# Kernel tuning notes

Hardware: AMD Instinct MI355X
Metric: run time of the kernel (lower is better)

## Reference

```python
import jax, jax.numpy as jnp
import numpy as np

N = 100000
DIM = 128
E = 3200000


def setup_inputs() -> dict:
    key = jax.random.key(0)
    k1, k2, k3, k4 = jax.random.split(key, 4)
    x = jax.random.normal(k1, (N, DIM), dtype=jnp.float32)
    edge_index = jax.random.randint(k2, (2, E), 0, N, dtype=jnp.int64)
    # GCNConv params: glorot-style weight [dim, dim], zero-init bias
    W = jax.random.normal(k3, (DIM, DIM), dtype=jnp.float32) * (1.0 / np.sqrt(DIM))
    b = jnp.zeros((DIM,), dtype=jnp.float32)
    return {"x": x, "edge_index": edge_index, "W": W, "b": b}


def gcn_conv(x, edge_index, W, b):
    n = x.shape[0]
    # add self-loops (PyG default add_self_loops=True)
    loop = jnp.arange(n, dtype=edge_index.dtype)
    row = jnp.concatenate([edge_index[0], loop])  # source
    col = jnp.concatenate([edge_index[1], loop])  # target (aggregation index)
    # symmetric normalization D^-1/2 (A+I) D^-1/2; degree counted on targets
    deg = jax.ops.segment_sum(jnp.ones_like(col, dtype=x.dtype), col, num_segments=n)
    dinv = jnp.where(deg > 0, jax.lax.rsqrt(deg), 0.0)
    norm = dinv[row] * dinv[col]  # [E+N]
    xw = x @ W  # dense transform first (dim small)
    msgs = xw[row] * norm[:, None]  # gather + scale
    out = jax.ops.segment_sum(msgs, col, num_segments=n)  # scatter-add
    return out + b


def reference(x, edge_index, W, b):
    # NOTE: original torch loop recomputes from the same x every iteration,
    # so the result equals a single relu(GCNConv(x, edge_index)).
    return jax.nn.relu(gcn_conv(x, edge_index, W, b))
```

## Files before the change

kernel.cpp:

```cpp
#include <hip/hip_runtime.h>

#define DIM 128
#define E_FIXED 3200000
#define BSH 7
#define BNODES 128
#define NB 784
#define BCAP 4864
#define NBLK 256
#define CAPH 2816

__device__ __forceinline__ float bflo(unsigned int w) { return __uint_as_float(w << 16); }
__device__ __forceinline__ float bfhi(unsigned int w) { return __uint_as_float(w & 0xffff0000u); }
__device__ __forceinline__ unsigned short f2bf(float f) {
    union { float f; unsigned int u; } c; c.f = f;
    unsigned int u = c.u + 0x7FFFu + ((c.u >> 16) & 1u);
    return (unsigned short)(u >> 16);
}

__global__ void detect_kernel(const int* __restrict__ edge, int force64, int* __restrict__ flag) {
    __shared__ int any_nonzero;
    if (threadIdx.x == 0) any_nonzero = 0;
    __syncthreads();
    if (edge[2 * threadIdx.x + 1] != 0) atomicOr(&any_nonzero, 1);
    __syncthreads();
    if (threadIdx.x == 0) *flag = force64 ? 1 : (any_nonzero ? 0 : 1);
}

__global__ __launch_bounds__(1024) void hist_kernel(const int* __restrict__ edge,
                                                    const int* __restrict__ flag,
                                                    int* __restrict__ hist_g, int E) {
    __shared__ int h[NB];
    const int tid = threadIdx.x;
    const int k = blockIdx.x;
    for (int b = tid; b < NB; b += 1024) h[b] = 0;
    __syncthreads();

    const int sh = *flag;
    const int cpb = (E + NBLK - 1) / NBLK;
    const int e0 = k * cpb;
    const int e1 = min(E, e0 + cpb);
    for (int e = e0 + tid; e < e1; e += 1024) {
        int c = edge[((size_t)(E + e)) << sh];
        atomicAdd(&h[c >> BSH], 1);
    }
    __syncthreads();
    for (int b = tid; b < NB; b += 1024) hist_g[(size_t)k * NB + b] = h[b];
}

__global__ __launch_bounds__(NBLK) void prefix_kernel(const int* __restrict__ hist_g,
                                                      int* __restrict__ pre_t,
                                                      int* __restrict__ total) {
    __shared__ int sc[2][NBLK];
    const int b = blockIdx.x;
    const int t = threadIdx.x;
    int v = hist_g[(size_t)t * NB + b];
    sc[0][t] = v;
    __syncthreads();
    int buf = 0;
#pragma unroll
    for (int off = 1; off < NBLK; off <<= 1) {
        sc[buf ^ 1][t] = sc[buf][t] + ((t >= off) ? sc[buf][t - off] : 0);
        buf ^= 1;
        __syncthreads();
    }
    pre_t[(size_t)b * NBLK + t] = sc[buf][t] - v;
    if (t == NBLK - 1) total[b] = sc[buf][t];
}

__global__ __launch_bounds__(512) void scatter_kernel(const int* __restrict__ edge,
                                                      const int* __restrict__ flag,
                                                      const int* __restrict__ pre_t,
                                                      int* __restrict__ bucketed, int E) {
    __shared__ int cur[NB];
    const int tid = threadIdx.x;
    const int k = blockIdx.x;
    for (int b = tid; b < NB; b += 512) cur[b] = pre_t[(size_t)b * NBLK + k];
    __syncthreads();

    const int sh = *flag;
    const int cpb = (E + NBLK - 1) / NBLK;
    const int e0 = k * cpb;
    const int e1 = min(E, e0 + cpb);
    for (int e = e0 + tid; e < e1; e += 512) {
        int r = edge[((size_t)e) << sh];
        int c = edge[((size_t)(E + e)) << sh];
        int b = c >> BSH;
        int pos = atomicAdd(&cur[b], 1);
        if (pos < BCAP)
            bucketed[(size_t)b * BCAP + pos] = (r << BSH) | (c & (BNODES - 1));
    }
}

__global__ __launch_bounds__(256) void degree_kernel(const int* __restrict__ bucketed,
                                                     const int* __restrict__ total,
                                                     int* __restrict__ deg, int n) {
    __shared__ int h[BNODES];
    const int b = blockIdx.x, t = threadIdx.x;
    if (t < BNODES) h[t] = 0;
    __syncthreads();
    const int m = min(total[b], BCAP);
    const int* seg = bucketed + (size_t)b * BCAP;
    for (int i = t; i < m; i += 256) atomicAdd(&h[seg[i] & (BNODES - 1)], 1);
    __syncthreads();
    int gnode = (b << BSH) + t;
    if (t < BNODES && gnode < n) deg[gnode] = h[t];
}

__global__ __launch_bounds__(256) void gemm_kernel(const float* __restrict__ x,
                                                   const float* __restrict__ W,
                                                   const int* __restrict__ deg,
                                                   unsigned short* __restrict__ xws, int n) {
    __shared__ float xs[64][132];
    const int tid = threadIdx.x;
    const int base = blockIdx.x * 64;
#pragma unroll
    for (int it = 0; it < 8; ++it) {
        int idx = it * 256 + tid;
        int r = idx >> 5;
        int k4 = idx & 31;
        int gr = base + r;
        float4 v = make_float4(0.f, 0.f, 0.f, 0.f);
        if (gr < n) v = ((const float4*)(x + (size_t)gr * DIM))[k4];
        *(float4*)&xs[r][k4 * 4] = v;
    }
    __syncthreads();

    const int j = tid & 31;
    const int g = tid >> 5;
    const float4* W4 = (const float4*)W;
    float acc[8][4];
#pragma unroll
    for (int t = 0; t < 8; ++t) { acc[t][0] = acc[t][1] = acc[t][2] = acc[t][3] = 0.f; }

    for (int k0 = 0; k0 < DIM; k0 += 4) {
        float4 w0 = W4[(size_t)(k0 + 0) * 32 + j];
        float4 w1 = W4[(size_t)(k0 + 1) * 32 + j];
        float4 w2 = W4[(size_t)(k0 + 2) * 32 + j];
        float4 w3 = W4[(size_t)(k0 + 3) * 32 + j];
#pragma unroll
        for (int t = 0; t < 8; ++t) {
            float4 xv = *(const float4*)&xs[g * 8 + t][k0];
            acc[t][0] = fmaf(xv.x, w0.x, fmaf(xv.y, w1.x, fmaf(xv.z, w2.x, fmaf(xv.w, w3.x, acc[t][0]))));
            acc[t][1] = fmaf(xv.x, w0.y, fmaf(xv.y, w1.y, fmaf(xv.z, w2.y, fmaf(xv.w, w3.y, acc[t][1]))));
            acc[t][2] = fmaf(xv.x, w0.z, fmaf(xv.y, w1.z, fmaf(xv.z, w2.z, fmaf(xv.w, w3.z, acc[t][2]))));
            acc[t][3] = fmaf(xv.x, w0.w, fmaf(xv.y, w1.w, fmaf(xv.z, w2.w, fmaf(xv.w, w3.w, acc[t][3]))));
        }
    }
#pragma unroll
    for (int t = 0; t < 8; ++t) {
        int gr = base + g * 8 + t;
        if (gr < n) {
            float dv = rsqrtf((float)(deg[gr] + 1));
            ushort4 o;
            o.x = f2bf(acc[t][0] * dv); o.y = f2bf(acc[t][1] * dv);
            o.z = f2bf(acc[t][2] * dv); o.w = f2bf(acc[t][3] * dv);
            *(ushort4*)&xws[(size_t)gr * DIM + j * 4] = o;
        }
    }
}

__device__ __forceinline__ void bf8_acc(uint4 u, float4& p, float4& r) {
    p.x += bflo(u.x); p.y += bfhi(u.x);
    p.z += bflo(u.y); p.w += bfhi(u.y);
    r.x += bflo(u.z); r.y += bfhi(u.z);
    r.z += bflo(u.w); r.w += bfhi(u.w);
}

__global__ __launch_bounds__(256) void agg_kernel(const unsigned short* __restrict__ xws,
                                                  const int* __restrict__ bucketed,
                                                  const int* __restrict__ total,
                                                  const int* __restrict__ deg,
                                                  const float* __restrict__ bias,
                                                  float* __restrict__ out, int n) {
    __shared__ int lds_csr[CAPH];
    __shared__ int hcur[64];
    __shared__ int sc[2][64];
    __shared__ int loff[65];
    __shared__ float sdn[64];
    __shared__ float sbias[DIM];

    const int tid = threadIdx.x;
    const int b = blockIdx.x >> 1;
    const int half = blockIdx.x & 1;
    const int m = min(total[b], BCAP);
    const int* seg = bucketed + (size_t)b * BCAP;
    const int base_node = (b << BSH) + half * 64;

    if (tid < 64) {
        int gn = base_node + tid;
        int d = (gn < n) ? deg[gn] : 0;
        sc[0][tid] = d;
        hcur[tid] = 0;
        sdn[tid] = rsqrtf((float)(d + 1));
    }
    if (tid < DIM) sbias[tid] = bias[tid];
    __syncthreads();
    int buf = 0;
#pragma unroll
    for (int off = 1; off < 64; off <<= 1) {
        if (tid < 64)
            sc[buf ^ 1][tid] = sc[buf][tid] + ((tid >= off) ? sc[buf][tid - off] : 0);
        buf ^= 1;
        __syncthreads();
    }
    if (tid < 64) loff[tid + 1] = sc[buf][tid];
    if (tid == 0) loff[0] = 0;
    __syncthreads();

    for (int i = tid; i < m; i += 256) {
        int v = seg[i];
        int loc = v & (BNODES - 1);
        if ((loc >> 6) == half) {
            int pos = atomicAdd(&hcur[loc & 63], 1);
            lds_csr[loff[loc & 63] + pos] = v >> BSH;
        }
    }
    __syncthreads();

    const int wave = tid >> 6, lane = tid & 63;
    const int q = lane >> 4;
    const int l16 = lane & 15;
    const int d0 = l16 * 8;

    for (int nl = wave * 16; nl < wave * 16 + 16; ++nl) {
        int gnode = base_node + nl;
        if (gnode >= n) break;
        int s = loff[nl], epos = loff[nl + 1];

        float4 a0 = make_float4(0.f, 0.f, 0.f, 0.f), a1 = a0, b0 = a0, b1 = a0;
        if (q == 0) {
            uint4 u = *(const uint4*)&xws[(size_t)gnode * DIM + d0];
            bf8_acc(u, a0, a1);
        }

        int e = s;
        for (; e + 16 <= epos; e += 16) {
            int r0 = lds_csr[e + q];
            int r1 = lds_csr[e + 4 + q];
            int r2 = lds_csr[e + 8 + q];
            int r3 = lds_csr[e + 12 + q];
            uint4 u0 = *(const uint4*)&xws[(size_t)r0 * DIM + d0];
            uint4 u1 = *(const uint4*)&xws[(size_t)r1 * DIM + d0];
            uint4 u2 = *(const uint4*)&xws[(size_t)r2 * DIM + d0];
            uint4 u3 = *(const uint4*)&xws[(size_t)r3 * DIM + d0];
            bf8_acc(u0, a0, a1);
            bf8_acc(u1, b0, b1);
            bf8_acc(u2, a0, a1);
            bf8_acc(u3, b0, b1);
        }
        for (; e + 4 <= epos; e += 4) {
            int r0 = lds_csr[e + q];
            uint4 u0 = *(const uint4*)&xws[(size_t)r0 * DIM + d0];
            bf8_acc(u0, a0, a1);
        }
        for (; e < epos; ++e) {
            if (q == 0) {
                int r = lds_csr[e];
                uint4 u = *(const uint4*)&xws[(size_t)r * DIM + d0];
                bf8_acc(u, a0, a1);
            }
        }

        float t0x = a0.x + b0.x, t0y = a0.y + b0.y, t0z = a0.z + b0.z, t0w = a0.w + b0.w;
        float t1x = a1.x + b1.x, t1y = a1.y + b1.y, t1z = a1.z + b1.z, t1w = a1.w + b1.w;
        t0x += __shfl_xor(t0x, 16); t0y += __shfl_xor(t0y, 16);
        t0z += __shfl_xor(t0z, 16); t0w += __shfl_xor(t0w, 16);
        t1x += __shfl_xor(t1x, 16); t1y += __shfl_xor(t1y, 16);
        t1z += __shfl_xor(t1z, 16); t1w += __shfl_xor(t1w, 16);
        t0x += __shfl_xor(t0x, 32); t0y += __shfl_xor(t0y, 32);
        t0z += __shfl_xor(t0z, 32); t0w += __shfl_xor(t0w, 32);
        t1x += __shfl_xor(t1x, 32); t1y += __shfl_xor(t1y, 32);
        t1z += __shfl_xor(t1z, 32); t1w += __shfl_xor(t1w, 32);

        float dn = sdn[nl];
        if (q == 0) {
            float4 sb = *(const float4*)&sbias[d0];
            float4 o;
            o.x = fmaxf(t0x * dn + sb.x, 0.f);
            o.y = fmaxf(t0y * dn + sb.y, 0.f);
            o.z = fmaxf(t0z * dn + sb.z, 0.f);
            o.w = fmaxf(t0w * dn + sb.w, 0.f);
            *(float4*)&out[(size_t)gnode * DIM + d0] = o;
        } else if (q == 1) {
            float4 sb = *(const float4*)&sbias[d0 + 4];
            float4 o;
            o.x = fmaxf(t1x * dn + sb.x, 0.f);
            o.y = fmaxf(t1y * dn + sb.y, 0.f);
            o.z = fmaxf(t1z * dn + sb.z, 0.f);
            o.w = fmaxf(t1w * dn + sb.w, 0.f);
            *(float4*)&out[(size_t)gnode * DIM + d0 + 4] = o;
        }
    }
}

extern "C" void kernel_launch(void* const* d_in, const int* in_sizes, int n_in,
                              void* d_out, int out_size, void* d_ws, size_t ws_size,
                              hipStream_t stream) {
    const float* x    = (const float*)d_in[0];
    const int*   edge = (const int*)d_in[1];
    const float* W    = (const float*)d_in[2];
    const float* bias = (const float*)d_in[3];
    float* out = (float*)d_out;

    const int n = in_sizes[0] / DIM;
    const int E = (in_sizes[1] == 4 * E_FIXED) ? E_FIXED : in_sizes[1] / 2;
    const int force64 = (in_sizes[1] == 4 * E_FIXED) ? 1 : 0;
    const int nbuck = (n + BNODES - 1) >> BSH;
    const int nhalf = (n + 63) / 64;

    char* p = (char*)d_ws;
    auto carve = [&](size_t bytes) { char* r = p; p += (bytes + 255) & ~(size_t)255; return (void*)r; };
    unsigned short* xws = (unsigned short*)carve((size_t)n * DIM * 2);
    int*   deg      = (int*)carve((size_t)n * 4);
    int*   flag     = (int*)carve(256);
    int*   hist_g   = (int*)carve((size_t)NBLK * NB * 4);
    int*   pre_t    = (int*)carve((size_t)NB * NBLK * 4);
    int*   total    = (int*)carve((size_t)NB * 4);
    int*   bucketed = (int*)carve((size_t)NB * BCAP * 4);

    detect_kernel<<<1, 128, 0, stream>>>(edge, force64, flag);
    hist_kernel<<<NBLK, 1024, 0, stream>>>(edge, flag, hist_g, E);
    prefix_kernel<<<NB, NBLK, 0, stream>>>(hist_g, pre_t, total);
    scatter_kernel<<<NBLK, 512, 0, stream>>>(edge, flag, pre_t, bucketed, E);
    degree_kernel<<<nbuck, 256, 0, stream>>>(bucketed, total, deg, n);
    gemm_kernel<<<(n + 63) / 64, 256, 0, stream>>>(x, W, deg, xws, n);
    agg_kernel<<<nhalf * 2, 256, 0, stream>>>(xws, bucketed, total, deg, bias, out, n);
}
```

Before: 230.8 us.

## Shrink buckets to 64 nodes, inline edge-width detection, software-pipeline gathers

Buckets now cover 64 nodes instead of 128, so each aggregation block reads only its own bucket rather than scanning a shared bucket and discarding half the entries. The separate detect kernel and its flag buffer are removed; each block works out the edge index width itself with a wave ballot. The main gather loop is software-pipelined: the next 16 neighbour rows are loaded while the current ones are accumulated, to hide gather latency. The risks are more buckets for the histogram and prefix passes, a per-bucket capacity that may overflow on skewed degree distributions, and higher register pressure from the pipelining.

```diff
diff --git a/kernel.cpp b/kernel.cpp
--- a/kernel.cpp
+++ b/kernel.cpp
@@ -2,12 +2,11 @@
 
 #define DIM 128
 #define E_FIXED 3200000
-#define BSH 7
-#define BNODES 128
-#define NB 784
-#define BCAP 4864
+#define BSH 6
+#define BNODES 64
+#define NB 1600
+#define BCAP 2816
 #define NBLK 256
-#define CAPH 2816
 
 __device__ __forceinline__ float bflo(unsigned int w) { return __uint_as_float(w << 16); }
 __device__ __forceinline__ float bfhi(unsigned int w) { return __uint_as_float(w & 0xffff0000u); }
@@ -17,25 +16,22 @@
     return (unsigned short)(u >> 16);
 }
 
-__global__ void detect_kernel(const int* __restrict__ edge, int force64, int* __restrict__ flag) {
-    __shared__ int any_nonzero;
-    if (threadIdx.x == 0) any_nonzero = 0;
-    __syncthreads();
-    if (edge[2 * threadIdx.x + 1] != 0) atomicOr(&any_nonzero, 1);
-    __syncthreads();
-    if (threadIdx.x == 0) *flag = force64 ? 1 : (any_nonzero ? 0 : 1);
+__device__ __forceinline__ int edge_shift(const int* __restrict__ edge, int force64) {
+    int w = edge[2 * (threadIdx.x & 63) + 1];
+    unsigned long long nz = __ballot(w != 0);
+    return force64 ? 1 : (nz ? 0 : 1);
 }
 
 __global__ __launch_bounds__(1024) void hist_kernel(const int* __restrict__ edge,
-                                                    const int* __restrict__ flag,
+                                                    int force64,
                                                     int* __restrict__ hist_g, int E) {
     __shared__ int h[NB];
+    const int sh = edge_shift(edge, force64);
     const int tid = threadIdx.x;
     const int k = blockIdx.x;
     for (int b = tid; b < NB; b += 1024) h[b] = 0;
     __syncthreads();
 
-    const int sh = *flag;
     const int cpb = (E + NBLK - 1) / NBLK;
     const int e0 = k * cpb;
     const int e1 = min(E, e0 + cpb);
@@ -68,16 +64,16 @@
 }
 
 __global__ __launch_bounds__(512) void scatter_kernel(const int* __restrict__ edge,
-                                                      const int* __restrict__ flag,
+                                                      int force64,
                                                       const int* __restrict__ pre_t,
                                                       int* __restrict__ bucketed, int E) {
     __shared__ int cur[NB];
+    const int sh = edge_shift(edge, force64);
     const int tid = threadIdx.x;
     const int k = blockIdx.x;
     for (int b = tid; b < NB; b += 512) cur[b] = pre_t[(size_t)b * NBLK + k];
     __syncthreads();
 
-    const int sh = *flag;
     const int cpb = (E + NBLK - 1) / NBLK;
     const int e0 = k * cpb;
     const int e1 = min(E, e0 + cpb);
@@ -172,21 +168,20 @@
                                                   const int* __restrict__ deg,
                                                   const float* __restrict__ bias,
                                                   float* __restrict__ out, int n) {
-    __shared__ int lds_csr[CAPH];
-    __shared__ int hcur[64];
-    __shared__ int sc[2][64];
-    __shared__ int loff[65];
-    __shared__ float sdn[64];
+    __shared__ int lds_csr[BCAP];
+    __shared__ int hcur[BNODES];
+    __shared__ int sc[2][BNODES];
+    __shared__ int loff[BNODES + 1];
+    __shared__ float sdn[BNODES];
     __shared__ float sbias[DIM];
 
     const int tid = threadIdx.x;
-    const int b = blockIdx.x >> 1;
-    const int half = blockIdx.x & 1;
+    const int b = blockIdx.x;
     const int m = min(total[b], BCAP);
     const int* seg = bucketed + (size_t)b * BCAP;
-    const int base_node = (b << BSH) + half * 64;
-
-    if (tid < 64) {
+    const int base_node = b << BSH;
+
+    if (tid < BNODES) {
         int gn = base_node + tid;
         int d = (gn < n) ? deg[gn] : 0;
         sc[0][tid] = d;
@@ -197,23 +192,21 @@
     __syncthreads();
     int buf = 0;
 #pragma unroll
-    for (int off = 1; off < 64; off <<= 1) {
-        if (tid < 64)
+    for (int off = 1; off < BNODES; off <<= 1) {
+        if (tid < BNODES)
             sc[buf ^ 1][tid] = sc[buf][tid] + ((tid >= off) ? sc[buf][tid - off] : 0);
         buf ^= 1;
         __syncthreads();
     }
-    if (tid < 64) loff[tid + 1] = sc[buf][tid];
+    if (tid < BNODES) loff[tid + 1] = sc[buf][tid];
     if (tid == 0) loff[0] = 0;
     __syncthreads();
 
     for (int i = tid; i < m; i += 256) {
         int v = seg[i];
         int loc = v & (BNODES - 1);
-        if ((loc >> 6) == half) {
-            int pos = atomicAdd(&hcur[loc & 63], 1);
-            lds_csr[loff[loc & 63] + pos] = v >> BSH;
-        }
+        int pos = atomicAdd(&hcur[loc], 1);
+        lds_csr[loff[loc] + pos] = v >> BSH;
     }
     __syncthreads();
 
@@ -225,7 +218,7 @@
     for (int nl = wave * 16; nl < wave * 16 + 16; ++nl) {
         int gnode = base_node + nl;
         if (gnode >= n) break;
-        int s = loff[nl], epos = loff[nl + 1];
+        const int s0 = loff[nl], epos = loff[nl + 1];
 
         float4 a0 = make_float4(0.f, 0.f, 0.f, 0.f), a1 = a0, b0 = a0, b1 = a0;
         if (q == 0) {
@@ -233,20 +226,33 @@
             bf8_acc(u, a0, a1);
         }
 
-        int e = s;
-        for (; e + 16 <= epos; e += 16) {
-            int r0 = lds_csr[e + q];
-            int r1 = lds_csr[e + 4 + q];
-            int r2 = lds_csr[e + 8 + q];
-            int r3 = lds_csr[e + 12 + q];
-            uint4 u0 = *(const uint4*)&xws[(size_t)r0 * DIM + d0];
-            uint4 u1 = *(const uint4*)&xws[(size_t)r1 * DIM + d0];
-            uint4 u2 = *(const uint4*)&xws[(size_t)r2 * DIM + d0];
-            uint4 u3 = *(const uint4*)&xws[(size_t)r3 * DIM + d0];
-            bf8_acc(u0, a0, a1);
-            bf8_acc(u1, b0, b1);
-            bf8_acc(u2, a0, a1);
-            bf8_acc(u3, b0, b1);
+        const int ng = (epos - s0) >> 4;
+        uint4 c0, c1, c2, c3;
+        if (ng > 0) {
+            int r0 = lds_csr[s0 + q],      r1 = lds_csr[s0 + 4 + q];
+            int r2 = lds_csr[s0 + 8 + q],  r3 = lds_csr[s0 + 12 + q];
+            c0 = *(const uint4*)&xws[(size_t)r0 * DIM + d0];
+            c1 = *(const uint4*)&xws[(size_t)r1 * DIM + d0];
+            c2 = *(const uint4*)&xws[(size_t)r2 * DIM + d0];
+            c3 = *(const uint4*)&xws[(size_t)r3 * DIM + d0];
+        }
+        for (int g2 = 1; g2 < ng; ++g2) {
+            int eb = s0 + (g2 << 4);
+            int r0 = lds_csr[eb + q],      r1 = lds_csr[eb + 4 + q];
+            int r2 = lds_csr[eb + 8 + q],  r3 = lds_csr[eb + 12 + q];
+            uint4 n0 = *(const uint4*)&xws[(size_t)r0 * DIM + d0];
+            uint4 n1 = *(const uint4*)&xws[(size_t)r1 * DIM + d0];
+            uint4 n2 = *(const uint4*)&xws[(size_t)r2 * DIM + d0];
+            uint4 n3 = *(const uint4*)&xws[(size_t)r3 * DIM + d0];
+            bf8_acc(c0, a0, a1); bf8_acc(c1, b0, b1);
+            bf8_acc(c2, a0, a1); bf8_acc(c3, b0, b1);
+            c0 = n0; c1 = n1; c2 = n2; c3 = n3;
+        }
+        int e = s0;
+        if (ng > 0) {
+            bf8_acc(c0, a0, a1); bf8_acc(c1, b0, b1);
+            bf8_acc(c2, a0, a1); bf8_acc(c3, b0, b1);
+            e = s0 + (ng << 4);
         }
         for (; e + 4 <= epos; e += 4) {
             int r0 = lds_csr[e + q];
@@ -306,23 +312,20 @@
     const int E = (in_sizes[1] == 4 * E_FIXED) ? E_FIXED : in_sizes[1] / 2;
     const int force64 = (in_sizes[1] == 4 * E_FIXED) ? 1 : 0;
     const int nbuck = (n + BNODES - 1) >> BSH;
-    const int nhalf = (n + 63) / 64;
 
     char* p = (char*)d_ws;
     auto carve = [&](size_t bytes) { char* r = p; p += (bytes + 255) & ~(size_t)255; return (void*)r; };
     unsigned short* xws = (unsigned short*)carve((size_t)n * DIM * 2);
     int*   deg      = (int*)carve((size_t)n * 4);
-    int*   flag     = (int*)carve(256);
     int*   hist_g   = (int*)carve((size_t)NBLK * NB * 4);
     int*   pre_t    = (int*)carve((size_t)NB * NBLK * 4);
     int*   total    = (int*)carve((size_t)NB * 4);
     int*   bucketed = (int*)carve((size_t)NB * BCAP * 4);
 
-    detect_kernel<<<1, 128, 0, stream>>>(edge, force64, flag);
-    hist_kernel<<<NBLK, 1024, 0, stream>>>(edge, flag, hist_g, E);
-    prefix_kernel<<<NB, NBLK, 0, stream>>>(hist_g, pre_t, total);
-    scatter_kernel<<<NBLK, 512, 0, stream>>>(edge, flag, pre_t, bucketed, E);
+    hist_kernel<<<NBLK, 1024, 0, stream>>>(edge, force64, hist_g, E);
+    prefix_kernel<<<nbuck, NBLK, 0, stream>>>(hist_g, pre_t, total);
+    scatter_kernel<<<NBLK, 512, 0, stream>>>(edge, force64, pre_t, bucketed, E);
     degree_kernel<<<nbuck, 256, 0, stream>>>(bucketed, total, deg, n);
     gemm_kernel<<<(n + 63) / 64, 256, 0, stream>>>(x, W, deg, xws, n);
-    agg_kernel<<<nhalf * 2, 256, 0, stream>>>(xws, bucketed, total, deg, bias, out, n);
-}
+    agg_kernel<<<nbuck, 256, 0, stream>>>(xws, bucketed, total, deg, bias, out, n);
+}
```

Result: slower. 244.5 us (+5.9%).
